# Optimization experiments

Measured on AMD Instinct MI355X. Metric: run time of the kernel, lower is better.

Reference implementation:

```python
import jax, jax.numpy as jnp
import numpy as np

B, F, D = 1024, 39, 16
HIDDEN = [128, 128, 128]


def _cin(x, Ws, bs):
    # x: (B, F0, D) stacked field embeddings
    F0 = x.shape[1]
    h = x  # hidden_nn_layers[-1], shape (B, Fk, D)
    outs = []
    n = len(Ws)
    for i, (W, b) in enumerate(zip(Ws, bs)):
        L = W.shape[-1]
        Fk = h.shape[1]
        Wr = W.reshape(F0, Fk, L)  # conv1d kernel [1, F0*Fk, L] -> (F0, Fk, L)
        # per-embedding-dim field outer product: (B, F0, Fk, D)
        z = jnp.einsum('bfd,bgd->bfgd', x, h)
        # pointwise conv over D + bias + relu -> (B, L, D)
        cur = jax.nn.relu(jnp.einsum('bfgd,fgl->bld', z, Wr) + b[None, :, None])
        if i != n - 1:
            h = cur[:, : L // 2]          # next_hidden
            direct = cur[:, L // 2 :]     # direct_connect
        else:
            direct = cur
        outs.append(direct)
    # concat over field axis, sum over embedding dim -> (B, sum_direct)
    return jnp.concatenate(outs, axis=1).sum(-1)


def setup_inputs() -> dict:
    key = jax.random.key(0)
    ks = jax.random.split(key, 8)
    x = jax.random.normal(ks[0], (B, F, D), dtype=jnp.float32)
    field_nums = [F]
    Ws, bs = [], []
    for i, L in enumerate(HIDDEN):
        fan_in = field_nums[0] * field_nums[-1]
        lim = np.sqrt(6.0 / fan_in)  # he_uniform
        Ws.append(jax.random.uniform(ks[1 + i], (fan_in, L), jnp.float32, -lim, lim))
        bs.append(jnp.zeros((L,), jnp.float32))
        field_nums.append(L // 2)
    return {"x": x, "W0": Ws[0], "W1": Ws[1], "W2": Ws[2],
            "b0": bs[0], "b1": bs[1], "b2": bs[2]}


def reference(x, W0, W1, W2, b0, b1, b2):
    return _cin(x, [W0, W1, W2], [b0, b1, b2])
```

## Files before the change

kernel.cpp:

```cpp
#include <hip/hip_runtime.h>


#define NF     39
#define LCH    128
#define NLAYER 3
#define NFT    (NLAYER * NF)

typedef __bf16        bf16x8 __attribute__((ext_vector_type(8)));
typedef unsigned int  uint4v __attribute__((ext_vector_type(4)));
typedef float         f32x4  __attribute__((ext_vector_type(4)));

__device__ __forceinline__ unsigned short f2bf_rne(float f) {
    unsigned u = __float_as_uint(f);
    u += 0x7fffu + ((u >> 16) & 1u);
    return (unsigned short)(u >> 16);
}

__global__ void cin_prep(const float* __restrict__ W0,
                         const float* __restrict__ W1,
                         const float* __restrict__ W2,
                         unsigned short* __restrict__ wt)
{
    const int t = blockIdx.x * blockDim.x + threadIdx.x;
    if (t >= NFT * 1024) return;
    const int n  = t & 127;
    const int q  = (t >> 7) & 3;
    const int ks = (t >> 9) & 1;
    const int tl = t >> 10;
    const int l  = tl / NF;
    const int f  = tl - l * NF;
    const float* W = (l == 0) ? W0 : (l == 1) ? W1 : W2;

    unsigned short v[8];
    #pragma unroll
    for (int j = 0; j < 8; ++j) {
        const int g = ks * 32 + q * 8 + j;
        float w = 0.0f;
        if (l == 0) { if (g < NF) w = W[(f * NF + g) * LCH + n]; }
        else        { w = W[(f * 64 + g) * LCH + n]; }
        v[j] = f2bf_rne(w);
    }
    uint4v pv;
    #pragma unroll
    for (int i = 0; i < 4; ++i)
        pv[i] = (unsigned)v[2 * i] | ((unsigned)v[2 * i + 1] << 16);
    ((uint4v*)wt)[t] = pv;
}

__global__ __launch_bounds__(512, 2) void cin_mfma(
    const float* __restrict__ x,
    const unsigned short* __restrict__ wt,
    const float* __restrict__ b0p,
    const float* __restrict__ b1p,
    const float* __restrict__ b2p,
    float* __restrict__ out)
{
    __shared__ __align__(16) unsigned short hfrag[8 * 64 * 8];
    __shared__ float xf32[NF * 64];
    __shared__ float biasl[NLAYER * LCH];

    const int tid  = threadIdx.x;
    const int lane = tid & 63;
    const int w    = tid >> 6;
    const int q    = lane >> 4;
    const int c    = lane & 15;
    const int nc   = w * 16 + c;
    const int bb   = blockIdx.x * 4;

    {
        f32x4 z = {0.f, 0.f, 0.f, 0.f};
        ((f32x4*)hfrag)[tid] = z;
    }
    for (int t = tid; t < NLAYER * LCH; t += 512)
        biasl[t] = (t < 128) ? b0p[t] : (t < 256) ? b1p[t - 128] : b2p[t - 256];
    __syncthreads();

    for (int i = tid; i < 4 * NF * 16; i += 512) {
        const float v = x[bb * (NF * 16) + i];
        const int lb = i / (NF * 16);
        const int r  = i - lb * (NF * 16);
        const int f  = r >> 4;
        const int d  = r & 15;
        const int sl = lb * 16 + d;
        xf32[f * 64 + sl] = v;
        hfrag[((f >> 3) * 64 + sl) * 8 + (f & 7)] = f2bf_rne(v);
    }

    const unsigned short* wq = wt + (q * 128 + nc) * 8;

    bf16x8 c0 = *(const bf16x8*)(wq);
    bf16x8 c1 = *(const bf16x8*)(wq + 4096);
    bf16x8 n0 = *(const bf16x8*)(wq + 8192);
    bf16x8 n1 = *(const bf16x8*)(wq + 8192 + 4096);

    __syncthreads();

    #pragma unroll 1
    for (int l = 0; l < NLAYER; ++l) {
        bf16x8 a[2][4];
        #pragma unroll
        for (int ks = 0; ks < 2; ++ks)
            #pragma unroll
            for (int mt = 0; mt < 4; ++mt)
                a[ks][mt] = *(const bf16x8*)&hfrag[((ks * 4 + q) * 64 + mt * 16 + c) * 8];

        f32x4 cur[4];
        #pragma unroll
        for (int mt = 0; mt < 4; ++mt) cur[mt] = f32x4{0.f, 0.f, 0.f, 0.f};
        const f32x4 z = {0.f, 0.f, 0.f, 0.f};

        #pragma unroll 1
        for (int f = 0; f < NF; ++f) {
            const bf16x8 bv0 = c0;
            const bf16x8 bv1 = c1;

            #pragma unroll
            for (int mt = 0; mt < 4; ++mt) {
                f32x4 sv = __builtin_amdgcn_mfma_f32_16x16x32_bf16(a[0][mt], bv0, z,  0, 0, 0);
                sv       = __builtin_amdgcn_mfma_f32_16x16x32_bf16(a[1][mt], bv1, sv, 0, 0, 0);
                const f32x4 xr = *(const f32x4*)&xf32[f * 64 + mt * 16 + q * 4];
                #pragma unroll
                for (int r = 0; r < 4; ++r)
                    cur[mt][r] = fmaf(xr[r], sv[r], cur[mt][r]);
            }

            c0 = n0; c1 = n1;
            int pf = l * NF + f + 2; if (pf > NFT - 1) pf = NFT - 1;
            const unsigned short* p = wq + (size_t)pf * 8192;
            n0 = *(const bf16x8*)p;
            n1 = *(const bf16x8*)(p + 4096);
        }

        const float bias = biasl[l * LCH + nc];
        float v[4][4];
        #pragma unroll
        for (int mt = 0; mt < 4; ++mt)
            #pragma unroll
            for (int r = 0; r < 4; ++r)
                v[mt][r] = fmaxf(cur[mt][r] + bias, 0.f);

        if (l < 2 && w < 4) {
            #pragma unroll
            for (int mt = 0; mt < 4; ++mt)
                #pragma unroll
                for (int r = 0; r < 4; ++r)
                    hfrag[((nc >> 3) * 64 + mt * 16 + q * 4 + r) * 8 + (nc & 7)] =
                        f2bf_rne(v[mt][r]);
        } else {
            const int outcol = (l == 0) ? nc - 64 : (l == 1) ? nc : 128 + nc;
            #pragma unroll
            for (int mt = 0; mt < 4; ++mt) {
                float sacc = v[mt][0] + v[mt][1] + v[mt][2] + v[mt][3];
                sacc += __shfl_xor(sacc, 16, 64);
                sacc += __shfl_xor(sacc, 32, 64);
                if (lane < 16) out[(bb + mt) * 256 + outcol] = sacc;
            }
        }
        if (l < 2) __syncthreads();
    }
}

extern "C" void kernel_launch(void* const* d_in, const int* in_sizes, int n_in,
                              void* d_out, int out_size, void* d_ws, size_t ws_size,
                              hipStream_t stream) {
    const float* x  = (const float*)d_in[0];
    const float* W0 = (const float*)d_in[1];
    const float* W1 = (const float*)d_in[2];
    const float* W2 = (const float*)d_in[3];
    const float* b0 = (const float*)d_in[4];
    const float* b1 = (const float*)d_in[5];
    const float* b2 = (const float*)d_in[6];
    float* out = (float*)d_out;
    unsigned short* wt = (unsigned short*)d_ws;

    const int prep_threads = NFT * 1024;
    cin_prep<<<(prep_threads + 255) / 256, 256, 0, stream>>>(W0, W1, W2, wt);
    cin_mfma<<<256, 512, 0, stream>>>(x, wt, b0, b1, b2, out);
}
```

Measured before the change: 116.8 us.

## Fuse weight prep into main kernel via cooperative grid sync and unroll layer loop

```diff
diff --git a/kernel.cpp b/kernel.cpp
--- a/kernel.cpp
+++ b/kernel.cpp
@@ -1,10 +1,13 @@
 #include <hip/hip_runtime.h>
+#include <hip/hip_cooperative_groups.h>
+
+namespace cg = cooperative_groups;
 
 
 #define NF     39
 #define LCH    128
 #define NLAYER 3
-#define NFT    (NLAYER * NF)
+#define NFT    117
 
 typedef __bf16        bf16x8 __attribute__((ext_vector_type(8)));
 typedef unsigned int  uint4v __attribute__((ext_vector_type(4)));
@@ -16,40 +19,97 @@
     return (unsigned short)(u >> 16);
 }
 
-__global__ void cin_prep(const float* __restrict__ W0,
-                         const float* __restrict__ W1,
-                         const float* __restrict__ W2,
-                         unsigned short* __restrict__ wt)
+__device__ __forceinline__ void mfma_step(
+    const bf16x8 a00, const bf16x8 a01, const bf16x8 a02, const bf16x8 a03,
+    const bf16x8 a10, const bf16x8 a11, const bf16x8 a12, const bf16x8 a13,
+    const bf16x8 B0, const bf16x8 B1,
+    f32x4& cur0, f32x4& cur1, f32x4& cur2, f32x4& cur3,
+    const float* xrow, int q)
 {
-    const int t = blockIdx.x * blockDim.x + threadIdx.x;
-    if (t >= NFT * 1024) return;
-    const int n  = t & 127;
-    const int q  = (t >> 7) & 3;
-    const int ks = (t >> 9) & 1;
-    const int tl = t >> 10;
-    const int l  = tl / NF;
-    const int f  = tl - l * NF;
-    const float* W = (l == 0) ? W0 : (l == 1) ? W1 : W2;
-
-    unsigned short v[8];
+    const f32x4 z = {0.f, 0.f, 0.f, 0.f};
+    f32x4 s0 = __builtin_amdgcn_mfma_f32_16x16x32_bf16(a00, B0, z, 0, 0, 0);
+    f32x4 s1 = __builtin_amdgcn_mfma_f32_16x16x32_bf16(a01, B0, z, 0, 0, 0);
+    f32x4 s2 = __builtin_amdgcn_mfma_f32_16x16x32_bf16(a02, B0, z, 0, 0, 0);
+    f32x4 s3 = __builtin_amdgcn_mfma_f32_16x16x32_bf16(a03, B0, z, 0, 0, 0);
+    s0 = __builtin_amdgcn_mfma_f32_16x16x32_bf16(a10, B1, s0, 0, 0, 0);
+    s1 = __builtin_amdgcn_mfma_f32_16x16x32_bf16(a11, B1, s1, 0, 0, 0);
+    s2 = __builtin_amdgcn_mfma_f32_16x16x32_bf16(a12, B1, s2, 0, 0, 0);
+    s3 = __builtin_amdgcn_mfma_f32_16x16x32_bf16(a13, B1, s3, 0, 0, 0);
+    const f32x4 xr0 = *(const f32x4*)&xrow[ 0 + q * 4];
+    const f32x4 xr1 = *(const f32x4*)&xrow[16 + q * 4];
+    const f32x4 xr2 = *(const f32x4*)&xrow[32 + q * 4];
+    const f32x4 xr3 = *(const f32x4*)&xrow[48 + q * 4];
     #pragma unroll
-    for (int j = 0; j < 8; ++j) {
-        const int g = ks * 32 + q * 8 + j;
-        float w = 0.0f;
-        if (l == 0) { if (g < NF) w = W[(f * NF + g) * LCH + n]; }
-        else        { w = W[(f * 64 + g) * LCH + n]; }
-        v[j] = f2bf_rne(w);
-    }
-    uint4v pv;
-    #pragma unroll
-    for (int i = 0; i < 4; ++i)
-        pv[i] = (unsigned)v[2 * i] | ((unsigned)v[2 * i + 1] << 16);
-    ((uint4v*)wt)[t] = pv;
-}
-
-__global__ __launch_bounds__(512, 2) void cin_mfma(
+    for (int r = 0; r < 4; ++r) {
+        cur0[r] = fmaf(xr0[r], s0[r], cur0[r]);
+        cur1[r] = fmaf(xr1[r], s1[r], cur1[r]);
+        cur2[r] = fmaf(xr2[r], s2[r], cur2[r]);
+        cur3[r] = fmaf(xr3[r], s3[r], cur3[r]);
+    }
+}
+
+#define LOADB(B0, B1, TL)                                                     \
+    { int _t = (TL); if (_t > NFT - 1) _t = NFT - 1;                          \
+      const unsigned short* _p = wq + (size_t)_t * 8192;                      \
+      B0 = *(const bf16x8*)_p; B1 = *(const bf16x8*)(_p + 4096); }
+
+#define HSTORE(CUR, MT)                                                       \
+    { hfrag[((nc >> 3) * 64 + (MT) * 16 + q * 4 + 0) * 8 + (nc & 7)] =        \
+          f2bf_rne(fmaxf(CUR[0] + bias, 0.f));                                \
+      hfrag[((nc >> 3) * 64 + (MT) * 16 + q * 4 + 1) * 8 + (nc & 7)] =        \
+          f2bf_rne(fmaxf(CUR[1] + bias, 0.f));                                \
+      hfrag[((nc >> 3) * 64 + (MT) * 16 + q * 4 + 2) * 8 + (nc & 7)] =        \
+          f2bf_rne(fmaxf(CUR[2] + bias, 0.f));                                \
+      hfrag[((nc >> 3) * 64 + (MT) * 16 + q * 4 + 3) * 8 + (nc & 7)] =        \
+          f2bf_rne(fmaxf(CUR[3] + bias, 0.f)); }
+
+#define DSTORE(CUR, MT)                                                       \
+    { float sacc = fmaxf(CUR[0] + bias, 0.f) + fmaxf(CUR[1] + bias, 0.f)      \
+                 + fmaxf(CUR[2] + bias, 0.f) + fmaxf(CUR[3] + bias, 0.f);     \
+      sacc += __shfl_xor(sacc, 16, 64);                                       \
+      sacc += __shfl_xor(sacc, 32, 64);                                       \
+      if (lane < 16) out[(bb + (MT)) * 256 + outcol] = sacc; }
+
+#define LAYERBODY(L, FA0, FA1, FB0, FB1)                                      \
+  { const bf16x8 a00 = *(const bf16x8*)&hfrag[((0 + q) * 64 +  0 + c) * 8];   \
+    const bf16x8 a01 = *(const bf16x8*)&hfrag[((0 + q) * 64 + 16 + c) * 8];   \
+    const bf16x8 a02 = *(const bf16x8*)&hfrag[((0 + q) * 64 + 32 + c) * 8];   \
+    const bf16x8 a03 = *(const bf16x8*)&hfrag[((0 + q) * 64 + 48 + c) * 8];   \
+    const bf16x8 a10 = *(const bf16x8*)&hfrag[((4 + q) * 64 +  0 + c) * 8];   \
+    const bf16x8 a11 = *(const bf16x8*)&hfrag[((4 + q) * 64 + 16 + c) * 8];   \
+    const bf16x8 a12 = *(const bf16x8*)&hfrag[((4 + q) * 64 + 32 + c) * 8];   \
+    const bf16x8 a13 = *(const bf16x8*)&hfrag[((4 + q) * 64 + 48 + c) * 8];   \
+    f32x4 cur0 = {0,0,0,0}, cur1 = {0,0,0,0};                                 \
+    f32x4 cur2 = {0,0,0,0}, cur3 = {0,0,0,0};                                 \
+    int f = 0;                                                                \
+    _Pragma("unroll 1")                                                       \
+    for (int it = 0; it < 19; ++it) {                                         \
+        mfma_step(a00,a01,a02,a03,a10,a11,a12,a13, FA0, FA1,                  \
+                  cur0,cur1,cur2,cur3, &xf32[f * 64], q);                     \
+        LOADB(FA0, FA1, (L) * NF + f + 2);                                    \
+        mfma_step(a00,a01,a02,a03,a10,a11,a12,a13, FB0, FB1,                  \
+                  cur0,cur1,cur2,cur3, &xf32[(f + 1) * 64], q);               \
+        LOADB(FB0, FB1, (L) * NF + f + 3);                                    \
+        f += 2;                                                               \
+    }                                                                         \
+    mfma_step(a00,a01,a02,a03,a10,a11,a12,a13, FA0, FA1,                      \
+              cur0,cur1,cur2,cur3, &xf32[38 * 64], q);                        \
+    LOADB(FA0, FA1, (L) * NF + 40);                                           \
+    const float bias = ((L) == 0) ? biasv0 : ((L) == 1) ? biasv1 : biasv2;    \
+    if ((L) < 2 && w < 4) {                                                   \
+        HSTORE(cur0, 0) HSTORE(cur1, 1) HSTORE(cur2, 2) HSTORE(cur3, 3)       \
+    } else {                                                                  \
+        const int outcol = ((L) == 0) ? nc - 64 : ((L) == 1) ? nc : 128 + nc; \
+        DSTORE(cur0, 0) DSTORE(cur1, 1) DSTORE(cur2, 2) DSTORE(cur3, 3)       \
+    }                                                                         \
+    if ((L) < 2) __syncthreads(); }
+
+__global__ __launch_bounds__(512, 1) void cin_all(
     const float* __restrict__ x,
-    const unsigned short* __restrict__ wt,
+    const float* __restrict__ W0,
+    const float* __restrict__ W1,
+    const float* __restrict__ W2,
+    unsigned short* __restrict__ wt,
     const float* __restrict__ b0p,
     const float* __restrict__ b1p,
     const float* __restrict__ b2p,
@@ -57,7 +117,6 @@
 {
     __shared__ __align__(16) unsigned short hfrag[8 * 64 * 8];
     __shared__ float xf32[NF * 64];
-    __shared__ float biasl[NLAYER * LCH];
 
     const int tid  = threadIdx.x;
     const int lane = tid & 63;
@@ -68,13 +127,37 @@
     const int bb   = blockIdx.x * 4;
 
     {
-        f32x4 z = {0.f, 0.f, 0.f, 0.f};
-        ((f32x4*)hfrag)[tid] = z;
-    }
-    for (int t = tid; t < NLAYER * LCH; t += 512)
-        biasl[t] = (t < 128) ? b0p[t] : (t < 256) ? b1p[t - 128] : b2p[t - 256];
+        const int t = blockIdx.x * 512 + tid;
+        if (t < NFT * 1024) {
+            const int n  = t & 127;
+            const int qq = (t >> 7) & 3;
+            const int ks = (t >> 9) & 1;
+            const int tl = t >> 10;
+            const int l  = tl / NF;
+            const int f  = tl - l * NF;
+            const float* W = (l == 0) ? W0 : (l == 1) ? W1 : W2;
+            unsigned short v[8];
+            #pragma unroll
+            for (int j = 0; j < 8; ++j) {
+                const int g = ks * 32 + qq * 8 + j;
+                float wv = 0.0f;
+                if (l == 0) { if (g < NF) wv = W[(f * NF + g) * LCH + n]; }
+                else        { wv = W[(f * 64 + g) * LCH + n]; }
+                v[j] = f2bf_rne(wv);
+            }
+            uint4v pv;
+            #pragma unroll
+            for (int i = 0; i < 4; ++i)
+                pv[i] = (unsigned)v[2 * i] | ((unsigned)v[2 * i + 1] << 16);
+            ((uint4v*)wt)[t] = pv;
+        }
+    }
+
+    {
+        f32x4 zz = {0.f, 0.f, 0.f, 0.f};
+        ((f32x4*)hfrag)[tid] = zz;
+    }
     __syncthreads();
-
     for (int i = tid; i < 4 * NF * 16; i += 512) {
         const float v = x[bb * (NF * 16) + i];
         const int lb = i / (NF * 16);
@@ -85,79 +168,21 @@
         xf32[f * 64 + sl] = v;
         hfrag[((f >> 3) * 64 + sl) * 8 + (f & 7)] = f2bf_rne(v);
     }
+    const float biasv0 = b0p[nc];
+    const float biasv1 = b1p[nc];
+    const float biasv2 = b2p[nc];
+
+    cg::this_grid().sync();
 
     const unsigned short* wq = wt + (q * 128 + nc) * 8;
 
-    bf16x8 c0 = *(const bf16x8*)(wq);
-    bf16x8 c1 = *(const bf16x8*)(wq + 4096);
-    bf16x8 n0 = *(const bf16x8*)(wq + 8192);
-    bf16x8 n1 = *(const bf16x8*)(wq + 8192 + 4096);
-
-    __syncthreads();
-
-    #pragma unroll 1
-    for (int l = 0; l < NLAYER; ++l) {
-        bf16x8 a[2][4];
-        #pragma unroll
-        for (int ks = 0; ks < 2; ++ks)
-            #pragma unroll
-            for (int mt = 0; mt < 4; ++mt)
-                a[ks][mt] = *(const bf16x8*)&hfrag[((ks * 4 + q) * 64 + mt * 16 + c) * 8];
-
-        f32x4 cur[4];
-        #pragma unroll
-        for (int mt = 0; mt < 4; ++mt) cur[mt] = f32x4{0.f, 0.f, 0.f, 0.f};
-        const f32x4 z = {0.f, 0.f, 0.f, 0.f};
-
-        #pragma unroll 1
-        for (int f = 0; f < NF; ++f) {
-            const bf16x8 bv0 = c0;
-            const bf16x8 bv1 = c1;
-
-            #pragma unroll
-            for (int mt = 0; mt < 4; ++mt) {
-                f32x4 sv = __builtin_amdgcn_mfma_f32_16x16x32_bf16(a[0][mt], bv0, z,  0, 0, 0);
-                sv       = __builtin_amdgcn_mfma_f32_16x16x32_bf16(a[1][mt], bv1, sv, 0, 0, 0);
-                const f32x4 xr = *(const f32x4*)&xf32[f * 64 + mt * 16 + q * 4];
-                #pragma unroll
-                for (int r = 0; r < 4; ++r)
-                    cur[mt][r] = fmaf(xr[r], sv[r], cur[mt][r]);
-            }
-
-            c0 = n0; c1 = n1;
-            int pf = l * NF + f + 2; if (pf > NFT - 1) pf = NFT - 1;
-            const unsigned short* p = wq + (size_t)pf * 8192;
-            n0 = *(const bf16x8*)p;
-            n1 = *(const bf16x8*)(p + 4096);
-        }
-
-        const float bias = biasl[l * LCH + nc];
-        float v[4][4];
-        #pragma unroll
-        for (int mt = 0; mt < 4; ++mt)
-            #pragma unroll
-            for (int r = 0; r < 4; ++r)
-                v[mt][r] = fmaxf(cur[mt][r] + bias, 0.f);
-
-        if (l < 2 && w < 4) {
-            #pragma unroll
-            for (int mt = 0; mt < 4; ++mt)
-                #pragma unroll
-                for (int r = 0; r < 4; ++r)
-                    hfrag[((nc >> 3) * 64 + mt * 16 + q * 4 + r) * 8 + (nc & 7)] =
-                        f2bf_rne(v[mt][r]);
-        } else {
-            const int outcol = (l == 0) ? nc - 64 : (l == 1) ? nc : 128 + nc;
-            #pragma unroll
-            for (int mt = 0; mt < 4; ++mt) {
-                float sacc = v[mt][0] + v[mt][1] + v[mt][2] + v[mt][3];
-                sacc += __shfl_xor(sacc, 16, 64);
-                sacc += __shfl_xor(sacc, 32, 64);
-                if (lane < 16) out[(bb + mt) * 256 + outcol] = sacc;
-            }
-        }
-        if (l < 2) __syncthreads();
-    }
+    bf16x8 F0, F1, S0, S1;
+    LOADB(F0, F1, 0);
+    LOADB(S0, S1, 1);
+
+    LAYERBODY(0, F0, F1, S0, S1)
+    LAYERBODY(1, S0, S1, F0, F1)
+    LAYERBODY(2, F0, F1, S0, S1)
 }
 
 extern "C" void kernel_launch(void* const* d_in, const int* in_sizes, int n_in,
@@ -173,7 +198,8 @@
     float* out = (float*)d_out;
     unsigned short* wt = (unsigned short*)d_ws;
 
-    const int prep_threads = NFT * 1024;
-    cin_prep<<<(prep_threads + 255) / 256, 256, 0, stream>>>(W0, W1, W2, wt);
-    cin_mfma<<<256, 512, 0, stream>>>(x, wt, b0, b1, b2, out);
-}
+    void* args[] = { (void*)&x, (void*)&W0, (void*)&W1, (void*)&W2,
+                     (void*)&wt, (void*)&b0, (void*)&b1, (void*)&b2, (void*)&out };
+    hipLaunchCooperativeKernel((const void*)cin_all, dim3(256), dim3(512),
+                               args, 0, stream);
+}
```

After: 138.3 us. +18.5%, slower.
